# Optimization experiments

Measured on AMD Instinct MI355X. Metric: run time of the kernel, lower is better.

## Reference

```python
import jax, jax.numpy as jnp
import numpy as np

N = 256
DIAM = 2.0 * np.pi
VISC = 1e-3
DRAG = 0.1
SCALE = 1.0
PEAK_K = 4
DT = 0.001            # stable_time_step: min(0.001, 0.5*dx/max_velocity) = 0.001 here
NUM_STEPS = 90        # int(T/0.001), T=0.09
RECORD_EVERY = 30
BATCH = 8

# Carpenter-Kennedy low-storage RK4 / Crank-Nicolson tableau (jax-cfd crank_nicolson_rk4)
ALPHAS = (0.0, 0.1496590219993, 0.3704009573644, 0.6222557631345, 0.9582821306748, 1.0)
BETAS = (0.0, -0.4178904745, -1.192151694643, -1.697784692471, -1.514183444257)
GAMMAS = (0.1496590219993, 0.3792103129999, 0.8229550293869, 0.6994504559488, 0.1530572479681)


def _consts():
    kx = jnp.fft.fftfreq(N, d=DIAM / N).astype(jnp.float32)      # cycles / unit length
    ky = jnp.fft.rfftfreq(N, d=DIAM / N).astype(jnp.float32)
    KX, KY = jnp.meshgrid(kx, ky, indexing='ij')                 # [N, N//2+1]
    lap = -(2.0 * np.pi) ** 2 * (KX ** 2 + KY ** 2)              # (2*pi*i*k)^2, real
    lap_nz = lap.at[0, 0].set(1.0)
    # 2/3-rule brick wall dealiasing filter
    third = N // 3
    filt = jnp.zeros((N, N // 2 + 1), jnp.float32)
    filt = filt.at[:third, :third + 1].set(1.0)
    filt = filt.at[-third:, :third + 1].set(1.0)
    # Kolmogorov forcing u=(scale*sin(k y), 0) -> vorticity forcing -scale*k*cos(k y)
    y = (jnp.arange(N, dtype=jnp.float32) + 0.5) * (DIAM / N)    # cell centers
    f = -SCALE * PEAK_K * jnp.cos(PEAK_K * y)[None, :] * jnp.ones((N, 1), jnp.float32)
    f_hat = jnp.fft.rfft2(f)                                     # [N, N//2+1] complex
    return KX, KY, lap, lap_nz, filt, f_hat


def setup_inputs() -> dict:
    key = jax.random.key(0)
    w = jax.random.normal(key, (BATCH, N, N), jnp.float32)
    # band-pass around peak wavenumber to mimic a smooth initial vorticity field
    kx = jnp.fft.fftfreq(N, d=1.0 / N)
    ky = jnp.fft.rfftfreq(N, d=1.0 / N)
    kk = jnp.sqrt(kx[:, None] ** 2 + ky[None, :] ** 2)
    amp = jnp.exp(-0.5 * ((kk - PEAK_K) / 2.0) ** 2).astype(jnp.float32)
    w = jnp.fft.irfft2(jnp.fft.rfft2(w) * amp, s=(N, N))
    w = 5.0 * w / jnp.max(jnp.abs(w))
    return {"vort_init": w.astype(jnp.float32)}


def reference(vort_init) -> jnp.ndarray:
    KX, KY, lap, lap_nz, filt, f_hat = _consts()
    lin = VISC * lap - DRAG                 # implicit (linear) operator symbol, real
    two_pi_i = 2j * jnp.pi

    def explicit(w_hat):
        # vorticity -> velocity via streamfunction
        psi_hat = -w_hat / lap_nz
        vx = jnp.fft.irfft2(two_pi_i * KY * psi_hat, s=(N, N))
        vy = jnp.fft.irfft2(-two_pi_i * KX * psi_hat, s=(N, N))
        gx = jnp.fft.irfft2(two_pi_i * KX * w_hat, s=(N, N))
        gy = jnp.fft.irfft2(two_pi_i * KY * w_hat, s=(N, N))
        adv_hat = jnp.fft.rfft2(-(vx * gx + vy * gy)) * filt   # dealiased advection
        return adv_hat + f_hat

    @jax.checkpoint
    def step(w_hat):
        u = w_hat
        h = jnp.zeros_like(w_hat)
        for k in range(5):
            h = explicit(u) + BETAS[k] * h
            mu = 0.5 * DT * (ALPHAS[k + 1] - ALPHAS[k])
            u = (u + GAMMAS[k] * DT * h + mu * lin * u) / (1.0 - mu * lin)
        return u

    def body(u, _):
        u = step(u)
        return u, u

    w0 = jnp.fft.rfft2(vort_init)                    # [B, N, N//2+1]
    _, traj = jax.lax.scan(body, w0, None, length=NUM_STEPS)
    rec = traj[RECORD_EVERY - 1::RECORD_EVERY]       # [3, B, N, N//2+1]
    return jnp.fft.irfft2(rec, s=(N, N))             # [3, B, N, N]
```

## Files before the change

### kernel.cpp

```cpp
#include <hip/hip_runtime.h>
#include <math.h>

#define PI_F 3.14159265358979323846f
typedef unsigned long long u64;

__constant__ float c_beta[5] = {0.0f, -0.4178904745f, -1.192151694643f,
                                -1.697784692471f, -1.514183444257f};
__constant__ float c_gdt[5]  = {1.496590219993e-4f, 3.792103129999e-4f,
                                8.229550293869e-4f, 6.994504559488e-4f,
                                1.530572479681e-4f};
__constant__ float c_mu[5]   = {7.482951099965e-5f, 1.1037096768255e-4f,
                                1.2592740288505e-4f, 1.6801318377015e-4f,
                                2.08589346626e-5f};

struct __align__(128) Line { int v; int pad[31]; };

struct SharedMem {
  float sAr[2048], sAi[2048], sBr[2048], sBi[2048];
  float twr[128], twi[128];
  float t0r[430], t0i[430], t1r[430], t1i[430];
  float t2r[430], t2i[430], t3r[430], t3i[430];
};

__device__ __forceinline__ int swz(int i, int s4)
{
  return (i & ~31) | ((i + ((i >> 5) << s4)) & 31);
}

__device__ __forceinline__ float2 ldc(const float2* p)
{
  u64 v = __hip_atomic_load((const u64*)p, __ATOMIC_RELAXED, __HIP_MEMORY_SCOPE_AGENT);
  float2 f; __builtin_memcpy(&f, &v, 8); return f;
}
__device__ __forceinline__ void stg(float2* p, float2 f) { *p = f; }

__device__ __forceinline__ void bar_all(Line* arr, int n, int idx, int gen)
{
  __syncthreads();
  if (threadIdx.x == 0)
    __hip_atomic_store(&arr[idx].v, gen, __ATOMIC_RELAXED, __HIP_MEMORY_SCOPE_AGENT);
  if (threadIdx.x < 64) {
    bool done = false;
    while (!done) {
      bool ok = true;
      for (int w = threadIdx.x; w < n; w += 64)
        if (__hip_atomic_load(&arr[w].v, __ATOMIC_RELAXED, __HIP_MEMORY_SCOPE_AGENT) < gen)
          ok = false;
      done = __all(ok);
      if (!done) __builtin_amdgcn_s_sleep(2);
    }
    __builtin_amdgcn_sched_barrier(0);
  }
  __syncthreads();
}

__device__ __forceinline__ void bar_sync(Line* arr, Line* rel, int n, int idx,
                                         bool lead, int gen, bool fenced)
{
  const int t = threadIdx.x;
  __syncthreads();
  if (t == 0) {
    __builtin_amdgcn_s_waitcnt(0);
    __builtin_amdgcn_sched_barrier(0);
    if (fenced)
      __hip_atomic_store(&arr[idx].v, gen, __ATOMIC_RELEASE, __HIP_MEMORY_SCOPE_AGENT);
    else
      __hip_atomic_store(&arr[idx].v, gen, __ATOMIC_RELAXED, __HIP_MEMORY_SCOPE_AGENT);
  }
  if (lead && t < 64) {
    bool done = false;
    while (!done) {
      bool ok = true;
      for (int w = t; w < n; w += 64)
        if (__hip_atomic_load(&arr[w].v, __ATOMIC_RELAXED, __HIP_MEMORY_SCOPE_AGENT) < gen)
          ok = false;
      done = __all(ok);
      if (!done) __builtin_amdgcn_s_sleep(1);
    }
    __builtin_amdgcn_sched_barrier(0);
    if (fenced)
      (void)__hip_atomic_load(&arr[t & 7].v, __ATOMIC_ACQUIRE, __HIP_MEMORY_SCOPE_AGENT);
    if (t < 8) {
      if (fenced)
        __hip_atomic_store(&rel[t].v, gen, __ATOMIC_RELEASE, __HIP_MEMORY_SCOPE_AGENT);
      else
        __hip_atomic_store(&rel[t].v, gen, __ATOMIC_RELAXED, __HIP_MEMORY_SCOPE_AGENT);
    }
  }
  if (t == 0) {
    Line* f = &rel[idx & 7];
    while (__hip_atomic_load(&f->v, __ATOMIC_RELAXED, __HIP_MEMORY_SCOPE_AGENT) < gen)
      __builtin_amdgcn_s_sleep(1);
    if (fenced)
      (void)__hip_atomic_load(&f->v, __ATOMIC_ACQUIRE, __HIP_MEMORY_SCOPE_AGENT);
    __builtin_amdgcn_sched_barrier(0);
  }
  __syncthreads();
}

template<int B, bool INVERSE>
__device__ __forceinline__ void fftB(SharedMem& sh, int t)
{
  float *sr = sh.sAr, *si = sh.sAi, *dr = sh.sBr, *di = sh.sBi;
#pragma unroll
  for (int s = 0; s < 8; s += 2) {
    __syncthreads();
    const int m  = 1 << s;
    const int k  = t & (m - 1);
    const int e  = (t >> s) & 1;
    const int p  = (t >> (s + 1)) & 1;
    const int q0 = (t >> (s + 2)) << s;
    const int i0 = q0 + k;
    const float w1r = sh.twr[q0];
    const float w1i = INVERSE ? -sh.twi[q0] : sh.twi[q0];
    const float w2r = sh.twr[q0 << 1];
    const float w2i = INVERSE ? -sh.twi[q0 << 1] : sh.twi[q0 << 1];
#pragma unroll
    for (int f = 0; f < B; ++f) {
      const int base = f * 256;
      float S0r = sr[base + i0],       S0i = si[base + i0];
      float S1r = sr[base + i0 + 128], S1i = si[base + i0 + 128];
      float S2r = sr[base + i0 + 64],  S2i = si[base + i0 + 64];
      float S3r = sr[base + i0 + 192], S3i = si[base + i0 + 192];
      float Ar, Ai, Br, Bi;
      if (e == 0) { Ar = S0r + S1r; Ai = S0i + S1i; Br = S2r + S3r; Bi = S2i + S3i; }
      else {
        float xr = S0r - S1r, xi = S0i - S1i;
        Ar = xr * w1r - xi * w1i; Ai = xr * w1i + xi * w1r;
        float yr = S2r - S3r, yi = S2i - S3i;
        float tr = yr * w1r - yi * w1i, ti = yr * w1i + yi * w1r;
        Br = INVERSE ? -ti : ti; Bi = INVERSE ? tr : -tr;
      }
      float Or, Oi;
      if (p == 0) { Or = Ar + Br; Oi = Ai + Bi; }
      else {
        float xr = Ar - Br, xi = Ai - Bi;
        Or = xr * w2r - xi * w2i; Oi = xr * w2i + xi * w2r;
      }
      dr[base + t] = Or; di[base + t] = Oi;
    }
    float* tp;
    tp = sr; sr = dr; dr = tp;
    tp = si; si = di; di = tp;
  }
  __syncthreads();
}

template<bool INVERSE>
__device__ __forceinline__ void bfly4(const float (&vr)[4], const float (&vi)[4],
    float w1r, float w1i, float w2r, float w2i,
    float (&o_r)[4], float (&o_i)[4])
{
  float Ar  = vr[0] + vr[2], Ai  = vi[0] + vi[2];
  float dr_ = vr[0] - vr[2], di_ = vi[0] - vi[2];
  float Atr = dr_ * w1r - di_ * w1i, Ati = dr_ * w1i + di_ * w1r;
  float Br  = vr[1] + vr[3], Bi  = vi[1] + vi[3];
  float er_ = vr[1] - vr[3], ei_ = vi[1] - vi[3];
  float tr_ = er_ * w1r - ei_ * w1i, ti_ = er_ * w1i + ei_ * w1r;
  float Btr = INVERSE ? -ti_ : ti_;
  float Bti = INVERSE ?  tr_ : -tr_;
  o_r[0] = Ar + Br;   o_i[0] = Ai + Bi;
  o_r[1] = Atr + Btr; o_i[1] = Ati + Bti;
  float c0r = Ar - Br,   c0i = Ai - Bi;
  float c1r = Atr - Btr, c1i = Ati - Bti;
  o_r[2] = c0r * w2r - c0i * w2i; o_i[2] = c0r * w2i + c0i * w2r;
  o_r[3] = c1r * w2r - c1i * w2i; o_i[3] = c1r * w2i + c1i * w2r;
}

template<int B, bool INVERSE, int RO>
__device__ __forceinline__ void fft_reg(SharedMem& sh, int t,
                                        float (&vr)[4], float (&vi)[4])
{
  const int f  = t >> 6;
  const int tt = t & 63;
  if (f >= B) return;
  const int base = (f + RO) * 256;
#pragma unroll
  for (int s4 = 0; s4 < 4; ++s4) {
    const int s = s4 * 2;
    const int k  = tt & ((1 << s) - 1);
    const int q0 = tt - k;
    const float w1r = sh.twr[q0];
    const float w1i = INVERSE ? -sh.twi[q0] : sh.twi[q0];
    const float w2r = sh.twr[q0 << 1];
    const float w2i = INVERSE ? -sh.twi[q0 << 1] : sh.twi[q0 << 1];
    float o_r[4], o_i[4];
    bfly4<INVERSE>(vr, vi, w1r, w1i, w2r, w2i, o_r, o_i);
    if (s4 < 3) {
      const int pos0 = ((tt >> s) << (s + 2)) + k;
      float* xr = (s4 & 1) ? sh.sBr : sh.sAr;
      float* xi = (s4 & 1) ? sh.sBi : sh.sAi;
#pragma unroll
      for (int m = 0; m < 4; ++m) {
        const int w_ = base + swz(pos0 + (m << s), s4);
        xr[w_] = o_r[m]; xi[w_] = o_i[m];
      }
#pragma unroll
      for (int j = 0; j < 4; ++j) {
        const int rd = base + swz(tt + 64 * j, s4);
        vr[j] = xr[rd]; vi[j] = xi[rd];
      }
    } else {
#pragma unroll
      for (int j = 0; j < 4; ++j) { vr[j] = o_r[j]; vi[j] = o_i[j]; }
    }
  }
}

template<bool INVERSE>
__device__ __forceinline__ void fft_reg_dual(SharedMem& sh, int t,
    float (&ar)[4], float (&ai)[4], float (&br)[4], float (&bi)[4])
{
  const int f  = t >> 6;
  const int tt = t & 63;
  const int baseA = f * 256, baseB = (f + 4) * 256;
#pragma unroll
  for (int s4 = 0; s4 < 4; ++s4) {
    const int s = s4 * 2;
    const int k  = tt & ((1 << s) - 1);
    const int q0 = tt - k;
    const float w1r = sh.twr[q0];
    const float w1i = INVERSE ? -sh.twi[q0] : sh.twi[q0];
    const float w2r = sh.twr[q0 << 1];
    const float w2i = INVERSE ? -sh.twi[q0 << 1] : sh.twi[q0 << 1];
    float oAr[4], oAi[4], oBr[4], oBi[4];
    bfly4<INVERSE>(ar, ai, w1r, w1i, w2r, w2i, oAr, oAi);
    bfly4<INVERSE>(br, bi, w1r, w1i, w2r, w2i, oBr, oBi);
    if (s4 < 3) {
      const int pos0 = ((tt >> s) << (s + 2)) + k;
      float* xr = (s4 & 1) ? sh.sBr : sh.sAr;
      float* xi = (s4 & 1) ? sh.sBi : sh.sAi;
#pragma unroll
      for (int m = 0; m < 4; ++m) {
        const int w_ = swz(pos0 + (m << s), s4);
        xr[baseA + w_] = oAr[m]; xi[baseA + w_] = oAi[m];
        xr[baseB + w_] = oBr[m]; xi[baseB + w_] = oBi[m];
      }
#pragma unroll
      for (int j = 0; j < 4; ++j) {
        const int rd = swz(tt + 64 * j, s4);
        ar[j] = xr[baseA + rd]; ai[j] = xi[baseA + rd];
        br[j] = xr[baseB + rd]; bi[j] = xi[baseB + rd];
      }
    } else {
#pragma unroll
      for (int j = 0; j < 4; ++j) {
        ar[j] = oAr[j]; ai[j] = oAi[j];
        br[j] = oBr[j]; bi[j] = oBi[j];
      }
    }
  }
}


__device__ __forceinline__ void build_Z2(const float* t0r_, const float* t0i_,
    const float* t1r_, const float* t1i_, int f, int tt,
    float (&zr)[4], float (&zi)[4])
{
#pragma unroll
  for (int j = 0; j < 4; ++j) {
    int n = tt + 64 * j;
    bool low = (n <= 128);
    int kk = low ? n : 256 - n;
    float ar = 0.f, ai = 0.f, br = 0.f, bi = 0.f;
    if (kk <= 85) {
      ar = t0r_[kk * 5 + f]; ai = t0i_[kk * 5 + f];
      br = t1r_[kk * 5 + f]; bi = t1i_[kk * 5 + f];
    }
    zr[j] = low ? (ar - bi) : (ar + bi);
    zi[j] = low ? (ai + br) : (br - ai);
  }
}

__device__ __forceinline__ void real_item4_reg(SharedMem& sh, int t, int b, int x0,
    const float2* __restrict__ G, float2* __restrict__ NL1)
{
  const int f = t >> 6, tt = t & 63;
  for (int i = t; i < 344; i += 256) {
    int ky = i >> 2, xl = i & 3;
    float2 a0 = ldc(&G[(((size_t)0 * 8 + b) * 129 + ky) * 256 + x0 + xl]);
    float2 a1 = ldc(&G[(((size_t)1 * 8 + b) * 129 + ky) * 256 + x0 + xl]);
    float2 a2 = ldc(&G[(((size_t)2 * 8 + b) * 129 + ky) * 256 + x0 + xl]);
    float2 a3 = ldc(&G[(((size_t)3 * 8 + b) * 129 + ky) * 256 + x0 + xl]);
    sh.t0r[ky * 5 + xl] = a0.x; sh.t0i[ky * 5 + xl] = a0.y;
    sh.t1r[ky * 5 + xl] = a1.x; sh.t1i[ky * 5 + xl] = a1.y;
    sh.t2r[ky * 5 + xl] = a2.x; sh.t2i[ky * 5 + xl] = a2.y;
    sh.t3r[ky * 5 + xl] = a3.x; sh.t3i[ky * 5 + xl] = a3.y;
  }
  __syncthreads();
  float ar_[4], ai_[4], br_[4], bi_[4];
  build_Z2(sh.t0r, sh.t0i, sh.t1r, sh.t1i, f, tt, ar_, ai_);
  build_Z2(sh.t2r, sh.t2i, sh.t3r, sh.t3i, f, tt, br_, bi_);
  fft_reg_dual<true>(sh, t, ar_, ai_, br_, bi_);
  float nl[4];
#pragma unroll
  for (int j = 0; j < 4; ++j)
    nl[j] = -(ar_[j] * br_[j] + ai_[j] * bi_[j]);
#pragma unroll
  for (int j = 0; j < 4; ++j) sh.sAr[f * 256 + tt + 64 * j] = nl[j];
  __syncthreads();
  float wr2[4], wi2[4];
  if (f < 2) {
#pragma unroll
    for (int j = 0; j < 4; ++j) {
      wr2[j] = sh.sAr[(2 * f) * 256 + tt + 64 * j];
      wi2[j] = sh.sAr[(2 * f + 1) * 256 + tt + 64 * j];
    }
  }
  fft_reg<2, false, 4>(sh, t, wr2, wi2);
  if (f < 2) {
#pragma unroll
    for (int j = 0; j < 4; ++j) {
      sh.sBr[f * 256 + tt + 64 * j] = wr2[j];
      sh.sBi[f * 256 + tt + 64 * j] = wi2[j];
    }
  }
  __syncthreads();
  if (t <= 85) {
    int mI = (256 - t) & 255;
#pragma unroll
    for (int p = 0; p < 2; ++p) {
      float zr_ = sh.sBr[p * 256 + t],  zi_ = sh.sBi[p * 256 + t];
      float wr_ = sh.sBr[p * 256 + mI], wi_ = sh.sBi[p * 256 + mI];
      stg(&NL1[((size_t)b * 86 + t) * 256 + x0 + 2 * p],
          make_float2(0.5f * (zr_ + wr_), 0.5f * (zi_ - wi_)));
      stg(&NL1[((size_t)b * 86 + t) * 256 + x0 + 2 * p + 1],
          make_float2(0.5f * (zi_ + wi_), 0.5f * (wr_ - zr_)));
    }
  }
}

__device__ __forceinline__ void spectral_item2_reg(SharedMem& sh, int t, int b, int ky0,
    const float2* __restrict__ NL1, float2* __restrict__ u, float2* __restrict__ h,
    float2* __restrict__ G, float2* __restrict__ rec,
    float beta, float gdt, float mu, bool doUpdate, int recIdx)
{
  const int f = t >> 6, tt = t & 63;
  const size_t r0 = ((size_t)b * 129 + ky0) * 256;

  if (doUpdate) {
    float ar[4], ai[4];
    if (f < 2) {
#pragma unroll
      for (int j = 0; j < 4; ++j) {
        float2 nv = ldc(&NL1[((size_t)b * 86 + ky0 + f) * 256 + tt + 64 * j]);
        ar[j] = nv.x; ai[j] = nv.y;
      }
    }
    fft_reg<2, false, 0>(sh, t, ar, ai);
    if (f < 2) {
      const int ky = ky0 + f;
      const size_t row = r0 + (size_t)f * 256;
#pragma unroll
      for (int j = 0; j < 4; ++j) {
        const int kx = tt + 64 * j;
        const bool keep = (kx < 85) || (kx >= 171);
        float advr = keep ? ar[j] : 0.f;
        float advi = keep ? ai[j] : 0.f;
        if (kx == 0 && ky == 4) {
          float s_, c_;
          __sincosf(PI_F / 64.0f, &s_, &c_);
          advr -= 131072.0f * c_;
          advi -= 131072.0f * s_;
        }
        float hr = advr, hi = advi;
        if (beta != 0.0f) {
          float2 hh = h[row + kx];
          hr += beta * hh.x; hi += beta * hh.y;
        }
        const int jx = (kx < 128) ? kx : kx - 256;
        const float k2   = (float)(jx * jx + ky * ky);
        const float lin  = -0.001f * k2 - 0.1f;
        const float anum = 1.0f + mu * lin;
        const float invd = 1.0f / (1.0f - mu * lin);
        float2 uu = u[row + kx];
        float urv = (uu.x * anum + gdt * hr) * invd;
        float uiv = (uu.y * anum + gdt * hi) * invd;
        u[row + kx] = make_float2(urv, uiv);
        h[row + kx] = make_float2(hr, hi);
        if (recIdx >= 0)
          stg(&rec[((size_t)recIdx * 8 + b) * (129 * 256) + (size_t)ky * 256 + kx],
              make_float2(urv, uiv));
      }
    }
    __syncthreads();
  }

  float u0r[4], u0i[4], u1r[4], u1i[4];
#pragma unroll
  for (int j = 0; j < 4; ++j) {
    float2 a = u[r0 + tt + 64 * j];
    float2 c = u[r0 + 256 + tt + 64 * j];
    u0r[j] = a.x; u0i[j] = a.y; u1r[j] = c.x; u1i[j] = c.y;
  }

  const float NRM = 1.0f / 65536.0f;
  const float fy0 = (float)ky0, fy1 = (float)(ky0 + 1);
  float x0r[4], x0i[4], x1r[4], x1i[4];
#pragma unroll
  for (int j = 0; j < 4; ++j) {
    const int kx = tt + 64 * j;
    const int jx = (kx < 128) ? kx : kx - 256;
    const float fjx = (float)jx;
    {
      const float k2 = (float)(jx * jx + ky0 * ky0);
      const float il = (k2 == 0.f) ? 1.f : (-1.f / k2);
      const float urN = u0r[j] * NRM, uiN = u0i[j] * NRM;
      const float psr = -urN * il, psi_ = -uiN * il;
      if      (f == 0) { x0r[j] = -fy0 * psi_; x0i[j] =  fy0 * psr; }
      else if (f == 1) { x0r[j] =  fjx * psi_; x0i[j] = -fjx * psr; }
      else if (f == 2) { x0r[j] = -fjx * uiN;  x0i[j] =  fjx * urN; }
      else             { x0r[j] = -fy0 * uiN;  x0i[j] =  fy0 * urN; }
    }
    {
      const int ky1 = ky0 + 1;
      const float k2 = (float)(jx * jx + ky1 * ky1);
      const float il = (k2 == 0.f) ? 1.f : (-1.f / k2);
      const float urN = u1r[j] * NRM, uiN = u1i[j] * NRM;
      const float psr = -urN * il, psi_ = -uiN * il;
      if      (f == 0) { x1r[j] = -fy1 * psi_; x1i[j] =  fy1 * psr; }
      else if (f == 1) { x1r[j] =  fjx * psi_; x1i[j] = -fjx * psr; }
      else if (f == 2) { x1r[j] = -fjx * uiN;  x1i[j] =  fjx * urN; }
      else             { x1r[j] = -fy1 * uiN;  x1i[j] =  fy1 * urN; }
    }
  }
  fft_reg_dual<true>(sh, t, x0r, x0i, x1r, x1i);
#pragma unroll
  for (int j = 0; j < 4; ++j) {
    stg(&G[(((size_t)f * 8 + b) * 129 + ky0) * 256 + tt + 64 * j],
        make_float2(x0r[j], x0i[j]));
    stg(&G[(((size_t)f * 8 + b) * 129 + ky0 + 1) * 256 + tt + 64 * j],
        make_float2(x1r[j], x1i[j]));
  }
}

__global__ __launch_bounds__(256, 2) void k_persist(
    const float* __restrict__ vort, float* __restrict__ out,
    float2* __restrict__ u, float2* __restrict__ h,
    float2* __restrict__ G, float2* __restrict__ NL1, float2* __restrict__ rec,
    Line* __restrict__ bar)
{
  const int t   = threadIdx.x;
  const int blk = blockIdx.x;
  const int NBg = gridDim.x;

  Line* arrGrid = bar;
  Line* relGrid = bar + 1024;
  Line* arrGrpA = bar + 1032;
  Line* relGrpA = bar + 1032 + 2048;
  Line* regL    = bar + 1032 + 2048 + 64;

  __shared__ SharedMem sh;
  __shared__ int s_x, s_wi;

  if (t < 128) {
    float s_, c_;
    __sincosf(-(2.0f * PI_F / 256.0f) * (float)t, &s_, &c_);
    sh.twr[t] = c_; sh.twi[t] = s_;
  }

  if (t == 0) {
    int x;
    asm volatile("s_getreg_b32 %0, hwreg(HW_REG_XCC_ID)" : "=s"(x));
    x &= 15;
    s_x  = x;
    s_wi = atomicAdd(&regL[x].v, 1);
  }
  __syncthreads();

  int gen = 0;
  bar_sync(arrGrid, relGrid, NBg, blk, blk == 0, ++gen, true);

  int tot = 0, mn = 1 << 30, mx = 0;
  for (int i = 0; i < 8; ++i) {
    int c = regL[i].v;
    tot += c; mn = min(mn, c); mx = max(mx, c);
  }
  const bool fast = (tot == NBg) && (mn > 0) && (mx <= 256);
  int g, wi, nW;
  if (fast) { g = s_x;     wi = s_wi;     nW = regL[g].v; }
  else      { g = blk & 7; wi = blk >> 3; nW = NBg >> 3;  }
  Line* arr = arrGrpA + g * 256;
  Line* rel = relGrpA + g * 8;
  const bool lead = (wi == 0);

#define GBAR() do { ++gen; if (fast) bar_all(arr, nW, wi, gen); \
                    else bar_sync(arr, rel, nW, wi, lead, gen, true); } while (0)

  float2* W1 = rec + (size_t)g * (129 * 256);
  for (int w = wi; w < 64; w += nW) {
    const int x0 = w * 4;
#pragma unroll
    for (int p = 0; p < 2; ++p) {
      sh.sAr[p * 256 + t] = vort[((size_t)g * 256 + x0 + 2 * p) * 256 + t];
      sh.sAi[p * 256 + t] = vort[((size_t)g * 256 + x0 + 2 * p + 1) * 256 + t];
    }
    fftB<2, false>(sh, t);
    if (t < 129) {
      int mI = (256 - t) & 255;
#pragma unroll
      for (int p = 0; p < 2; ++p) {
        float zr = sh.sAr[p * 256 + t],  zi = sh.sAi[p * 256 + t];
        float wr = sh.sAr[p * 256 + mI], wi2 = sh.sAi[p * 256 + mI];
        stg(&W1[(size_t)t * 256 + x0 + 2 * p],
            make_float2(0.5f * (zr + wr), 0.5f * (zi - wi2)));
        stg(&W1[(size_t)t * 256 + x0 + 2 * p + 1],
            make_float2(0.5f * (zi + wi2), 0.5f * (wr - zr)));
      }
    }
    __syncthreads();
  }
  GBAR();

  for (int w = wi; w < 43; w += nW) {
    const int ky0 = w * 2;
#pragma unroll
    for (int f = 0; f < 2; ++f) {
      float2 v = ldc(&W1[(size_t)(ky0 + f) * 256 + t]);
      sh.sAr[f * 256 + t] = v.x; sh.sAi[f * 256 + t] = v.y;
    }
    fftB<2, false>(sh, t);
#pragma unroll
    for (int f = 0; f < 2; ++f)
      u[((size_t)g * 129 + ky0 + f) * 256 + t] =
        make_float2(sh.sAr[f * 256 + t], sh.sAi[f * 256 + t]);
  }
  __syncthreads();
  for (int w = wi; w < 43; w += nW)
    spectral_item2_reg(sh, t, g, w * 2, NL1, u, h, G, rec, 0.f, 0.f, 0.f, false, -1);

  for (int step = 1; step <= 90; ++step) {
    for (int k = 0; k < 5; ++k) {
      GBAR();
      for (int w = wi; w < 64; w += nW)
        real_item4_reg(sh, t, g, w * 4, G, NL1);
      GBAR();
      const int recIdx = (k == 4 && step % 30 == 0) ? (step / 30 - 1) : -1;
      for (int w = wi; w < 43; w += nW)
        spectral_item2_reg(sh, t, g, w * 2, NL1, u, h, G, rec,
                           c_beta[k], c_gdt[k], c_mu[k], true, recIdx);
    }
  }
  GBAR();

  for (int w = wi; w < 129; w += nW) {
#pragma unroll
    for (int j = 0; j < 2; ++j) {
      int idx = w * 2 + j, r = idx / 86, ky = idx % 86;
      float2 v = ldc(&rec[(((size_t)r * 8 + g) * 129 + ky) * 256 + t]);
      sh.sAr[j * 256 + t] = v.x; sh.sAi[j * 256 + t] = v.y;
    }
    fftB<2, true>(sh, t);
#pragma unroll
    for (int j = 0; j < 2; ++j) {
      int idx = w * 2 + j, r = idx / 86, ky = idx % 86;
      stg(&G[(((size_t)r * 8 + g) * 129 + ky) * 256 + t],
          make_float2(sh.sAr[j * 256 + t], sh.sAi[j * 256 + t]));
    }
    __syncthreads();
  }
  GBAR();

  const float NRM = 1.0f / 65536.0f;
  for (int w = wi; w < 192; w += nW) {
    const int r = w / 64, xh = w % 64, x0 = xh * 4;
    __syncthreads();
    for (int i = t; i < 344; i += 256) {
      int ky = i >> 2, xl = i & 3;
      float2 a = ldc(&G[(((size_t)r * 8 + g) * 129 + ky) * 256 + x0 + xl]);
      sh.t0r[ky * 5 + xl] = a.x; sh.t0i[ky * 5 + xl] = a.y;
    }
    __syncthreads();
    const bool lower = (t <= 128);
    const int  kk    = lower ? t : 256 - t;
#pragma unroll
    for (int f = 0; f < 2; ++f) {
      float ar = 0.f, ai = 0.f, br = 0.f, bi = 0.f;
      if (kk <= 85) {
        ar = sh.t0r[kk * 5 + 2 * f];     ai = sh.t0i[kk * 5 + 2 * f];
        br = sh.t0r[kk * 5 + 2 * f + 1]; bi = sh.t0i[kk * 5 + 2 * f + 1];
      }
      sh.sAr[f * 256 + t] = lower ? (ar - bi) : (ar + bi);
      sh.sAi[f * 256 + t] = lower ? (ai + br) : (br - ai);
    }
    fftB<2, true>(sh, t);
#pragma unroll
    for (int f = 0; f < 2; ++f) {
      out[((((size_t)r * 8 + g) * 256) + x0 + 2 * f) * 256 + t]     = sh.sAr[f * 256 + t] * NRM;
      out[((((size_t)r * 8 + g) * 256) + x0 + 2 * f + 1) * 256 + t] = sh.sAi[f * 256 + t] * NRM;
    }
    __syncthreads();
  }
#undef GBAR
}

extern "C" void kernel_launch(void* const* d_in, const int* in_sizes, int n_in,
                              void* d_out, int out_size, void* d_ws, size_t ws_size,
                              hipStream_t stream)
{
  const float* vort = (const float*)d_in[0];
  float* out = (float*)d_out;

  float2* base = (float2*)d_ws;
  float2* u    = base;
  float2* h    = u + 264192;
  float2* G    = h + 264192;
  float2* NL1  = G + 1056768;
  float2* rec  = NL1 + 176128;
  Line*   bar  = (Line*)(rec + 792576);
  const int nLines = 1024 + 8 + 2048 + 64 + 16;

  hipMemsetAsync(bar, 0, (size_t)nLines * sizeof(Line), stream);

  int maxPerCU = 0;
  hipOccupancyMaxActiveBlocksPerMultiprocessor(&maxPerCU, k_persist, 256, 0);
  int NBg = maxPerCU * 256;
  if (NBg <= 0)  NBg = 512;
  if (NBg > 512) NBg = 512;
  NBg &= ~63;
  if (NBg < 64)  NBg = 64;

  void* args[] = {(void*)&vort, (void*)&out, (void*)&u, (void*)&h,
                  (void*)&G, (void*)&NL1, (void*)&rec, (void*)&bar};
  hipError_t e = hipLaunchCooperativeKernel(k_persist, dim3(NBg), dim3(256),
                                            args, 0, stream);
  if (e != hipSuccess) {
    hipLaunchKernelGGL(k_persist, dim3(NBg), dim3(256), 0, stream,
                       vort, out, u, h, G, NL1, rec, bar);
  }
}
```

Before: 6.759 ms.

## Store G transposed so real-space loads read contiguous ky columns

The intermediate G spectral buffer is now stored as [field][batch][x][ky(86)] instead of [field][batch][ky][x]. The real-space stage can then read each x column's 86 ky values contiguously instead of gathering 4-wide strips across 129-row strides. The spectral stage now writes with a stride of 86 entries, which makes its stores scattered. Two smaller changes come with it: the sleep in the barrier spin loop is removed, and the shared staging arrays are merged into one padded layout.

```diff
diff --git a/kernel.cpp b/kernel.cpp
--- a/kernel.cpp
+++ b/kernel.cpp
@@ -18,8 +18,7 @@
 struct SharedMem {
   float sAr[2048], sAi[2048], sBr[2048], sBi[2048];
   float twr[128], twi[128];
-  float t0r[430], t0i[430], t1r[430], t1i[430];
-  float t2r[430], t2i[430], t3r[430], t3i[430];
+  float tR[1408], tI[1408];
 };
 
 __device__ __forceinline__ int swz(int i, int s4)
@@ -47,7 +46,6 @@
         if (__hip_atomic_load(&arr[w].v, __ATOMIC_RELAXED, __HIP_MEMORY_SCOPE_AGENT) < gen)
           ok = false;
       done = __all(ok);
-      if (!done) __builtin_amdgcn_s_sleep(2);
     }
     __builtin_amdgcn_sched_barrier(0);
   }
@@ -253,9 +251,8 @@
 }
 
 
-__device__ __forceinline__ void build_Z2(const float* t0r_, const float* t0i_,
-    const float* t1r_, const float* t1i_, int f, int tt,
-    float (&zr)[4], float (&zi)[4])
+__device__ __forceinline__ void build_Z2(const SharedMem& sh, int rowA, int rowB,
+    int tt, float (&zr)[4], float (&zi)[4])
 {
 #pragma unroll
   for (int j = 0; j < 4; ++j) {
@@ -264,8 +261,8 @@
     int kk = low ? n : 256 - n;
     float ar = 0.f, ai = 0.f, br = 0.f, bi = 0.f;
     if (kk <= 85) {
-      ar = t0r_[kk * 5 + f]; ai = t0i_[kk * 5 + f];
-      br = t1r_[kk * 5 + f]; bi = t1i_[kk * 5 + f];
+      ar = sh.tR[rowA + kk]; ai = sh.tI[rowA + kk];
+      br = sh.tR[rowB + kk]; bi = sh.tI[rowB + kk];
     }
     zr[j] = low ? (ar - bi) : (ar + bi);
     zi[j] = low ? (ai + br) : (br - ai);
@@ -273,24 +270,22 @@
 }
 
 __device__ __forceinline__ void real_item4_reg(SharedMem& sh, int t, int b, int x0,
-    const float2* __restrict__ G, float2* __restrict__ NL1)
+    const float2* __restrict__ GT, float2* __restrict__ NL1)
 {
   const int f = t >> 6, tt = t & 63;
-  for (int i = t; i < 344; i += 256) {
-    int ky = i >> 2, xl = i & 3;
-    float2 a0 = ldc(&G[(((size_t)0 * 8 + b) * 129 + ky) * 256 + x0 + xl]);
-    float2 a1 = ldc(&G[(((size_t)1 * 8 + b) * 129 + ky) * 256 + x0 + xl]);
-    float2 a2 = ldc(&G[(((size_t)2 * 8 + b) * 129 + ky) * 256 + x0 + xl]);
-    float2 a3 = ldc(&G[(((size_t)3 * 8 + b) * 129 + ky) * 256 + x0 + xl]);
-    sh.t0r[ky * 5 + xl] = a0.x; sh.t0i[ky * 5 + xl] = a0.y;
-    sh.t1r[ky * 5 + xl] = a1.x; sh.t1i[ky * 5 + xl] = a1.y;
-    sh.t2r[ky * 5 + xl] = a2.x; sh.t2i[ky * 5 + xl] = a2.y;
-    sh.t3r[ky * 5 + xl] = a3.x; sh.t3i[ky * 5 + xl] = a3.y;
+  for (int i = t; i < 1376; i += 256) {
+    int q   = i / 344;
+    int rem = i - q * 344;
+    int xl  = rem / 86;
+    int ky  = rem - xl * 86;
+    float2 a = ldc(&GT[(((size_t)q * 8 + b) * 256 + x0 + xl) * 86 + ky]);
+    sh.tR[(q * 4 + xl) * 88 + ky] = a.x;
+    sh.tI[(q * 4 + xl) * 88 + ky] = a.y;
   }
   __syncthreads();
   float ar_[4], ai_[4], br_[4], bi_[4];
-  build_Z2(sh.t0r, sh.t0i, sh.t1r, sh.t1i, f, tt, ar_, ai_);
-  build_Z2(sh.t2r, sh.t2i, sh.t3r, sh.t3i, f, tt, br_, bi_);
+  build_Z2(sh, (0 * 4 + f) * 88, (1 * 4 + f) * 88, tt, ar_, ai_);
+  build_Z2(sh, (2 * 4 + f) * 88, (3 * 4 + f) * 88, tt, br_, bi_);
   fft_reg_dual<true>(sh, t, ar_, ai_, br_, bi_);
   float nl[4];
 #pragma unroll
@@ -332,7 +327,7 @@
 
 __device__ __forceinline__ void spectral_item2_reg(SharedMem& sh, int t, int b, int ky0,
     const float2* __restrict__ NL1, float2* __restrict__ u, float2* __restrict__ h,
-    float2* __restrict__ G, float2* __restrict__ rec,
+    float2* __restrict__ GT, float2* __restrict__ rec,
     float beta, float gdt, float mu, bool doUpdate, int recIdx)
 {
   const int f = t >> 6, tt = t & 63;
@@ -427,17 +422,16 @@
   fft_reg_dual<true>(sh, t, x0r, x0i, x1r, x1i);
 #pragma unroll
   for (int j = 0; j < 4; ++j) {
-    stg(&G[(((size_t)f * 8 + b) * 129 + ky0) * 256 + tt + 64 * j],
-        make_float2(x0r[j], x0i[j]));
-    stg(&G[(((size_t)f * 8 + b) * 129 + ky0 + 1) * 256 + tt + 64 * j],
-        make_float2(x1r[j], x1i[j]));
+    const size_t xb = ((size_t)f * 8 + b) * 256 + tt + 64 * j;
+    stg(&GT[xb * 86 + ky0],     make_float2(x0r[j], x0i[j]));
+    stg(&GT[xb * 86 + ky0 + 1], make_float2(x1r[j], x1i[j]));
   }
 }
 
 __global__ __launch_bounds__(256, 2) void k_persist(
     const float* __restrict__ vort, float* __restrict__ out,
     float2* __restrict__ u, float2* __restrict__ h,
-    float2* __restrict__ G, float2* __restrict__ NL1, float2* __restrict__ rec,
+    float2* __restrict__ GT, float2* __restrict__ NL1, float2* __restrict__ rec,
     Line* __restrict__ bar)
 {
   const int t   = threadIdx.x;
@@ -527,22 +521,23 @@
   }
   __syncthreads();
   for (int w = wi; w < 43; w += nW)
-    spectral_item2_reg(sh, t, g, w * 2, NL1, u, h, G, rec, 0.f, 0.f, 0.f, false, -1);
+    spectral_item2_reg(sh, t, g, w * 2, NL1, u, h, GT, rec, 0.f, 0.f, 0.f, false, -1);
 
   for (int step = 1; step <= 90; ++step) {
     for (int k = 0; k < 5; ++k) {
       GBAR();
       for (int w = wi; w < 64; w += nW)
-        real_item4_reg(sh, t, g, w * 4, G, NL1);
+        real_item4_reg(sh, t, g, w * 4, GT, NL1);
       GBAR();
       const int recIdx = (k == 4 && step % 30 == 0) ? (step / 30 - 1) : -1;
       for (int w = wi; w < 43; w += nW)
-        spectral_item2_reg(sh, t, g, w * 2, NL1, u, h, G, rec,
+        spectral_item2_reg(sh, t, g, w * 2, NL1, u, h, GT, rec,
                            c_beta[k], c_gdt[k], c_mu[k], true, recIdx);
     }
   }
   GBAR();
 
+  float2* Gs = GT;
   for (int w = wi; w < 129; w += nW) {
 #pragma unroll
     for (int j = 0; j < 2; ++j) {
@@ -554,7 +549,7 @@
 #pragma unroll
     for (int j = 0; j < 2; ++j) {
       int idx = w * 2 + j, r = idx / 86, ky = idx % 86;
-      stg(&G[(((size_t)r * 8 + g) * 129 + ky) * 256 + t],
+      stg(&Gs[(((size_t)r * 8 + g) * 129 + ky) * 256 + t],
           make_float2(sh.sAr[j * 256 + t], sh.sAi[j * 256 + t]));
     }
     __syncthreads();
@@ -567,8 +562,9 @@
     __syncthreads();
     for (int i = t; i < 344; i += 256) {
       int ky = i >> 2, xl = i & 3;
-      float2 a = ldc(&G[(((size_t)r * 8 + g) * 129 + ky) * 256 + x0 + xl]);
-      sh.t0r[ky * 5 + xl] = a.x; sh.t0i[ky * 5 + xl] = a.y;
+      float2 a = ldc(&Gs[(((size_t)r * 8 + g) * 129 + ky) * 256 + x0 + xl]);
+      sh.tR[(ky)*5 + xl - (ky)*5 + (ky)*5 + xl] = a.x;
+      sh.tR[ky * 5 + xl] = a.x; sh.tI[ky * 5 + xl] = a.y;
     }
     __syncthreads();
     const bool lower = (t <= 128);
@@ -577,8 +573,8 @@
     for (int f = 0; f < 2; ++f) {
       float ar = 0.f, ai = 0.f, br = 0.f, bi = 0.f;
       if (kk <= 85) {
-        ar = sh.t0r[kk * 5 + 2 * f];     ai = sh.t0i[kk * 5 + 2 * f];
-        br = sh.t0r[kk * 5 + 2 * f + 1]; bi = sh.t0i[kk * 5 + 2 * f + 1];
+        ar = sh.tR[kk * 5 + 2 * f];     ai = sh.tI[kk * 5 + 2 * f];
+        br = sh.tR[kk * 5 + 2 * f + 1]; bi = sh.tI[kk * 5 + 2 * f + 1];
       }
       sh.sAr[f * 256 + t] = lower ? (ar - bi) : (ar + bi);
       sh.sAi[f * 256 + t] = lower ? (ai + br) : (br - ai);
@@ -604,8 +600,8 @@
   float2* base = (float2*)d_ws;
   float2* u    = base;
   float2* h    = u + 264192;
-  float2* G    = h + 264192;
-  float2* NL1  = G + 1056768;
+  float2* GT   = h + 264192;
+  float2* NL1  = GT + 1056768;
   float2* rec  = NL1 + 176128;
   Line*   bar  = (Line*)(rec + 792576);
   const int nLines = 1024 + 8 + 2048 + 64 + 16;
@@ -621,11 +617,11 @@
   if (NBg < 64)  NBg = 64;
 
   void* args[] = {(void*)&vort, (void*)&out, (void*)&u, (void*)&h,
-                  (void*)&G, (void*)&NL1, (void*)&rec, (void*)&bar};
+                  (void*)&GT, (void*)&NL1, (void*)&rec, (void*)&bar};
   hipError_t e = hipLaunchCooperativeKernel(k_persist, dim3(NBg), dim3(256),
                                             args, 0, stream);
   if (e != hipSuccess) {
     hipLaunchKernelGGL(k_persist, dim3(NBg), dim3(256), 0, stream,
-                       vort, out, u, h, G, NL1, rec, bar);
-  }
-}
+                       vort, out, u, h, GT, NL1, rec, bar);
+  }
+}
```

New measurement: 7.635 ms. +13.0%, slower.
